# Performance work log

Hardware: AMD Instinct MI355X
Metric: run time of the kernel (lower is better)

Reference implementation:

```python
import jax, jax.numpy as jnp
import numpy as np

B, F, L = 16384, 32, 64
FEAT, DOM, R = 100000, 8, 16
D_IN = F * L  # 2048
N_HIDDEN = 3  # hidden_units = [256, 128, 1]


def _p(k, shape, scale=0.05):
    return jax.random.normal(k, shape, dtype=jnp.float32) * scale


def setup_inputs() -> dict:
    key = jax.random.key(0)
    ks = jax.random.split(key, 32)
    return {
        'x': jax.random.randint(ks[0], (B, F), 0, FEAT),
        'd': jax.random.randint(ks[1], (B,), 0, DOM),
        'emb': _p(ks[2], (FEAT, L)),
        # share MLP: 2048 -> 1024 -> 512 (ReLU after each)
        'sW0': _p(ks[3], (D_IN, 1024)), 'sb0': _p(ks[4], (1024,)),
        'sW1': _p(ks[5], (1024, 512)), 'sb1': _p(ks[6], (512,)),
        # domain layer: 512 -> 256 shared kernel + per-domain LoRA
        'Dk0': _p(ks[7], (512, 256)), 'Db0': _p(ks[8], (256,)),
        'DA0': _p(ks[9], (DOM, 512, R)), 'DB0': _p(ks[10], (DOM, R, 256)), 'Dlb0': _p(ks[11], (DOM, 256)),
        # task layers: 256 -> 128 -> 1 shared kernels + per-task LoRA
        'Tk0': _p(ks[12], (256, 128)), 'Tb0': _p(ks[13], (128,)),
        'Tk1': _p(ks[14], (128, 1)), 'Tb1': _p(ks[15], (1,)),
        'TA0': _p(ks[16], (2, 256, R)), 'TB0': _p(ks[17], (2, R, 128)), 'Tlb0': _p(ks[18], (2, 128)),
        'TA1': _p(ks[19], (2, 128, R)), 'TB1': _p(ks[20], (2, R, 1)), 'Tlb1': _p(ks[21], (2, 1)),
        # gate hypernet + heads
        'gW0': _p(ks[22], (D_IN, 1024)), 'gb0': _p(ks[23], (1024,)),
        'gW1': _p(ks[24], (1024, 512)), 'gb1': _p(ks[25], (512,)),
        'h0W': _p(ks[26], (512, 4)), 'h0b': _p(ks[27], (4,)),
        'h1W': _p(ks[28], (512, 4)), 'h1b': _p(ks[29], (4,)),
    }


def _mlp2(x, W0, b0, W1, b1):
    return jax.nn.relu(jax.nn.relu(x @ W0 + b0) @ W1 + b1)


def _forward(x, d, emb, sW0, sb0, sW1, sb1, Dk0, Db0, DA0, DB0, Dlb0,
             Tk0, Tb0, Tk1, Tb1, TA0, TB0, Tlb0, TA1, TB1, Tlb1,
             gW0, gb0, gW1, gb1, h0W, h0b, h1W, h1b):
    x_emb = emb[x].reshape(x.shape[0], -1)          # (B, dnn_dim)
    x_dnn = _mlp2(x_emb, sW0, sb0, sW1, sb1)        # (B, 512)

    # ---- domain layer (i=0), k=0 -> ReLU applied ----
    share = x_dnn @ Dk0 + Db0                        # (B, 256)
    lora = jnp.einsum('bi,bir->br', x_dnn, DA0[d])   # per-sample domain LoRA gather+matmul
    lora = jnp.einsum('br,bro->bo', lora, DB0[d]) + Dlb0[d]
    d_dnn = jax.nn.relu(share + lora)                # activated
    # d_share / d_lora kept PRE-activation, as in source

    t_dnn = [d_dnn, d_dnn]
    t_share = [share, share]
    t_lora = [lora, lora]
    t_sl, t_ls = [], []
    Tk, Tb = [Tk0, Tk1], [Tb0, Tb1]
    TA, TB, Tlb = [TA0, TA1], [TB0, TB1], [Tlb0, Tlb1]

    k = 1  # shared counter, faithfully incremented per (i, t) step
    for i in range(2):
        for t in range(2):
            ds = t_dnn[t] @ Tk[i] + Tb[i]
            ss = t_share[t] @ Tk[i] + Tb[i]
            ls = t_lora[t] @ Tk[i] + Tb[i]
            t_ls.append(ls)
            A, Bm, lb = TA[i][t], TB[i][t], Tlb[i][t]
            dl = (t_dnn[t] @ A) @ Bm + lb[None, :]
            sl = (t_share[t] @ A) @ Bm + lb[None, :]
            ll = (t_lora[t] @ A) @ Bm + lb[None, :]
            t_dnn[t] = ds + dl
            t_share[t] = ss
            t_lora[t] = ll
            t_sl.append(sl)
            if k + 1 < N_HIDDEN:  # only fires at (i=0, t=0)
                t_dnn[t] = jax.nn.relu(t_dnn[t])
                t_share[t] = jax.nn.relu(t_share[t])
                t_lora[t] = jax.nn.relu(t_lora[t])
                t_sl[t] = jax.nn.relu(t_sl[t])
                t_ls[t] = jax.nn.relu(t_ls[t])
                k += 1

    # ---- gating (hypernet sees detached embedding) ----
    hyper = _mlp2(jax.lax.stop_gradient(x_emb), gW0, gb0, gW1, gb1)
    gates = [jax.nn.sigmoid(hyper @ h0W + h0b), jax.nn.sigmoid(hyper @ h1W + h1b)]

    outs = []
    for t in range(2):
        g = gates[t]
        # t_dnn/t_share/t_lora are (B,1); t_sl[t]/t_ls[t] are (B,128) from i=0 -> broadcast (B,128)
        outs.append(t_dnn[t] - g[:, 0:1] * t_share[t] - g[:, 1:2] * t_lora[t]
                    - g[:, 2:3] * t_sl[t] - g[:, 3:4] * t_ls[t])
    return jnp.stack(outs)  # (2, B, 128)


def reference(x, d, emb, sW0, sb0, sW1, sb1, Dk0, Db0, DA0, DB0, Dlb0,
              Tk0, Tb0, Tk1, Tb1, TA0, TB0, Tlb0, TA1, TB1, Tlb1,
              gW0, gb0, gW1, gb1, h0W, h0b, h1W, h1b):
    return _forward(x, d, emb, sW0, sb0, sW1, sb1, Dk0, Db0, DA0, DB0, Dlb0,
                    Tk0, Tb0, Tk1, Tb1, TA0, TB0, Tlb0, TA1, TB1, Tlb1,
                    gW0, gb0, gW1, gb1, h0W, h0b, h1W, h1b)
```

## Files before the change

kernel.cpp:

```cpp
#include <hip/hip_runtime.h>
#include <hip/hip_bf16.h>

#define BATCH 16384

typedef __attribute__((ext_vector_type(4))) float f32x4;
typedef __attribute__((ext_vector_type(8))) short bf16x8;

__device__ inline float b2f(unsigned short u) {
    union { unsigned u; float f; } c; c.u = ((unsigned)u) << 16; return c.f;
}
__device__ inline unsigned short f2b(float f) {
    __hip_bfloat16 h = __float2bfloat16(f);
    return *(unsigned short*)&h;
}

#define GLL16(g, l)                                                            \
    __builtin_amdgcn_global_load_lds(                                          \
        (const __attribute__((address_space(1))) void*)(g),                    \
        (__attribute__((address_space(3))) void*)(l), 16, 0, 0)

__global__ __launch_bounds__(256) void k_prep(
    const float* __restrict__ sW0, const float* __restrict__ gW0,
    const float* __restrict__ sW1, const float* __restrict__ gW1,
    const float* __restrict__ Dk0, const float* __restrict__ Tk0,
    const float* __restrict__ TA0,
    const float* __restrict__ sb0, const float* __restrict__ gb0,
    const float* __restrict__ sb1, const float* __restrict__ gb1,
    const float* __restrict__ Tb0, const float* __restrict__ DA0,
    const float* __restrict__ DB0, const float* __restrict__ emb,
    unsigned short* __restrict__ W1t, unsigned short* __restrict__ W2cat,
    unsigned short* __restrict__ Dk0t, unsigned short* __restrict__ Tcat,
    float* __restrict__ b1cat, float* __restrict__ b2cat, float* __restrict__ tb0c,
    unsigned short* __restrict__ DA0b, unsigned short* __restrict__ DB0b,
    unsigned short* __restrict__ embB)
{
    int id = blockIdx.x;
    const int tid = threadIdx.x;
    __shared__ float t[32][33];
    auto tcvt = [&](const float* src, int K, int N, unsigned short* dst,
                    int dst_off, int dst_ld, int bx, int by) {
        int k0 = by * 32, n0 = bx * 32;
        int tx = tid & 31, ty = tid >> 5;
        #pragma unroll
        for (int s = 0; s < 32; s += 8) {
            int k = k0 + ty + s, n = n0 + tx;
            t[ty + s][tx] = (k < K && n < N) ? src[(size_t)k * N + n] : 0.f;
        }
        __syncthreads();
        #pragma unroll
        for (int s = 0; s < 32; s += 8) {
            int n = n0 + ty + s, k = k0 + tx;
            if (n < N && k < K)
                dst[(size_t)(dst_off + n) * dst_ld + k] = f2b(t[tx][ty + s]);
        }
    };
    if (id < 4096) { int z = id >> 11, rem = id & 2047;
        tcvt(z ? gW0 : sW0, 2048, 1024, W1t, z * 1024, 2048, rem & 31, rem >> 5); return; }
    id -= 4096;
    if (id < 1024) { int z = id >> 9, rem = id & 511;
        tcvt(z ? gW1 : sW1, 1024, 512, W2cat, z * 512, 1024, rem & 15, rem >> 4); return; }
    id -= 1024;
    if (id < 128) { tcvt(Dk0, 512, 256, Dk0t, 0, 512, id & 7, id >> 3); return; }
    id -= 128;
    if (id < 32)  { tcvt(Tk0, 256, 128, Tcat, 0, 256, id & 3, id >> 2); return; }
    id -= 32;
    if (id < 16)  { int z = id >> 3;
        tcvt(TA0 + z * 256 * 16, 256, 16, Tcat, 128 + z * 16, 256, 0, id & 7); return; }
    id -= 16;
    if (id < 397) {
        int i = id * 256 + tid;
        if (i < 1024)            { b1cat[i] = sb0[i]; return; }
        if (i < 2048)            { b1cat[i] = gb0[i - 1024]; return; }
        if (i < 2560)            { b2cat[i - 2048] = sb1[i - 2048]; return; }
        if (i < 3072)            { b2cat[i - 2560 + 512] = gb1[i - 2560]; return; }
        if (i < 3200)            { tb0c[i - 3072] = Tb0[i - 3072]; return; }
        if (i < 3232)            { tb0c[i - 3200 + 128] = 0.f; return; }
        i -= 3232;
        if (i < 65536)           { DA0b[i] = f2b(DA0[i]); return; }
        i -= 65536;
        if (i < 32768)           { DB0b[i] = f2b(DB0[i]); return; }
        return;
    }
    id -= 397;
    {
        int e = (id * 256 + tid) * 4;
        if (e < 100000 * 64) {
            float4 v = *(const float4*)(emb + e);
            ushort4 o = { f2b(v.x), f2b(v.y), f2b(v.z), f2b(v.w) };
            *(ushort4*)(embB + e) = o;
        }
    }
}

template<int RELU, int OUTBF16, int GATHER>
__global__ __launch_bounds__(512, 2) void k_gemm256(
    const unsigned short* __restrict__ A, int lda, long Az,
    const unsigned short* __restrict__ Bt, int K, long Bz,
    const float* __restrict__ bias, int biasz,
    void* __restrict__ C, int ldc, long Cz,
    int N, const int* __restrict__ xsrc, const unsigned short* __restrict__ embB)
{
    extern __shared__ char smem_raw[];
    const int NT = K >> 6;
    const int tid  = threadIdx.x;
    const int lane = tid & 63;
    const int w    = tid >> 6;
    const int wr   = w >> 2, wc = w & 3;
    const int frow = lane & 15, kg = lane >> 4;
    const int z = blockIdx.z;
    A    += (size_t)z * Az;
    Bt   += (size_t)z * Bz;
    bias += (size_t)z * biasz;

    const int gx  = gridDim.x;
    const int nwg = gx * gridDim.y;
    const int lin = blockIdx.y * gx + blockIdx.x;
    const int qq  = nwg >> 3;
    const int swz = (lin & 7) * qq + (lin >> 3);
    const int bx = swz % gx, by = swz / gx;
    const int row0 = by * 256, col0 = bx * 256;

    const int lch = (lane & 7) ^ ((lane >> 3) & 7);
    const int isA = (lch < 4);
    const int eoBase = lch * 8;
    int* xbT = (int*)(smem_raw + 131072);
    int rrh[4];
    const unsigned short* gsrc[4];
    #pragma unroll
    for (int h = 0; h < 4; ++h) {
        int rr = h * 64 + w * 8 + (lane >> 3);
        rrh[h] = rr;
        if (isA) gsrc[h] = GATHER ? embB : A + (size_t)(row0 + rr) * lda + lch * 8;
        else     gsrc[h] = Bt + (size_t)min(col0 + rr, N - 1) * K + (lch - 4) * 8;
    }
    const int dBase = w * 1024;

    const int pA = (kg ^ (frow & 7)) * 16;
    const int pB = ((4 + kg) ^ (frow & 7)) * 16;
    int aOff[8], bOff[4];
    #pragma unroll
    for (int m = 0; m < 8; ++m) aOff[m] = (wr * 128 + m * 16 + frow) * 128 + pA;
    #pragma unroll
    for (int n = 0; n < 4; ++n) bOff[n] = (wc * 64 + n * 16 + frow) * 128 + pB;

#define STAGE(t_, ks_, slot_) do {                                              \
        int tc_ = min((int)(t_), NT - 1);                                       \
        int o_ = tc_ * 64 + (ks_) * 32;                                         \
        char* d_ = smem_raw + (slot_) * 65536 + (ks_) * 32768 + dBase;          \
        GLL16(gsrc[0] + o_, d_);                                                \
        GLL16(gsrc[1] + o_, d_ + 8192);                                         \
        GLL16(gsrc[2] + o_, d_ + 16384);                                        \
        GLL16(gsrc[3] + o_, d_ + 24576);                                        \
    } while (0)
#define STAGEX(ix_, tcb_, ks_, slot_) do {                                      \
        char* d_ = smem_raw + (slot_) * 65536 + (ks_) * 32768 + dBase;          \
        _Pragma("unroll")                                                       \
        for (int h_ = 0; h_ < 4; ++h_) {                                        \
            const unsigned short* sa_ = embB + (size_t)(ix_)[h_] * 64           \
                                        + (ks_) * 32 + eoBase;                  \
            const unsigned short* sb2_ = gsrc[h_] + (tcb_) * 64 + (ks_) * 32;   \
            GLL16(isA ? sa_ : sb2_, d_ + h_ * 8192);                            \
        }                                                                       \
    } while (0)
#define READS(sb_, ks_) do {                                                    \
        _Pragma("unroll")                                                       \
        for (int n = 0; n < 4; ++n)                                             \
            bfr[n] = *(const bf16x8*)(smem_raw + (sb_) + (ks_) * 32768 + bOff[n]); \
        _Pragma("unroll")                                                       \
        for (int mi = 0; mi < 8; ++mi)                                          \
            afr[mi] = *(const bf16x8*)(smem_raw + (sb_) + (ks_) * 32768 + aOff[mi]); \
    } while (0)
#define MFMA32() do {                                                           \
        __builtin_amdgcn_s_setprio(1);                                          \
        _Pragma("unroll")                                                       \
        for (int mi = 0; mi < 8; ++mi)                                          \
            _Pragma("unroll")                                                   \
            for (int n = 0; n < 4; ++n)                                         \
                acc[mi][n] = __builtin_amdgcn_mfma_f32_16x16x32_bf16(           \
                    bfr[n], afr[mi], acc[mi][n], 0, 0, 0);                      \
        __builtin_amdgcn_s_setprio(0);                                          \
    } while (0)
#define VM4   asm volatile("s_waitcnt vmcnt(4)" ::: "memory")
#define BARM  asm volatile("s_barrier" ::: "memory")

    f32x4 acc[8][4] = {};
    bf16x8 afr[8], bfr[4];
    int ixc[4] = {0, 0, 0, 0};

    if (GATHER) {
        const char* xs = (const char*)(xsrc + row0 * 32);
        #pragma unroll
        for (int r = 0; r < 4; ++r)
            GLL16(xs + r * 8192 + w * 1024 + lane * 16,
                  smem_raw + 65536 + r * 8192 + w * 1024);
        asm volatile("s_waitcnt vmcnt(0)" ::: "memory");
        BARM;
        const int* xlin = (const int*)(smem_raw + 65536);
        #pragma unroll
        for (int r = 0; r < 4; ++r) {
            int i = (r * 512 + tid) * 4;
            int rr_ = i >> 5, tc_ = i & 31;
            int4 vv = *(const int4*)(xlin + i);
            xbT[(tc_ + 0) * 256 + (rr_ ^ ((tc_ + 0) & 31))] = vv.x;
            xbT[(tc_ + 1) * 256 + (rr_ ^ ((tc_ + 1) & 31))] = vv.y;
            xbT[(tc_ + 2) * 256 + (rr_ ^ ((tc_ + 2) & 31))] = vv.z;
            xbT[(tc_ + 3) * 256 + (rr_ ^ ((tc_ + 3) & 31))] = vv.w;
        }
        asm volatile("s_waitcnt lgkmcnt(0)" ::: "memory");
        BARM;
        int ix0[4];
        #pragma unroll
        for (int h = 0; h < 4; ++h) ix0[h] = xbT[rrh[h]];
        STAGEX(ix0, 0, 0, 0); STAGEX(ix0, 0, 1, 0);
        int t1 = min(1, NT - 1);
        #pragma unroll
        for (int h = 0; h < 4; ++h) ixc[h] = xbT[t1 * 256 + (rrh[h] ^ (t1 & 31))];
    } else {
        STAGE(0, 0, 0); STAGE(0, 1, 0);
    }
    VM4; BARM;

    for (int t = 0; t < NT; ++t) {
        const int slot = t & 1, nslot = slot ^ 1;
        const int sb = slot * 65536;
        const int tcn = min(t + 1, NT - 1);
        int ixn[4];
        READS(sb, 0);
        if (GATHER) STAGEX(ixc, tcn, 0, nslot); else STAGE(t + 1, 0, nslot);
        if (GATHER) {
            int tc2 = min(t + 2, NT - 1);
            #pragma unroll
            for (int h = 0; h < 4; ++h) ixn[h] = xbT[tc2 * 256 + (rrh[h] ^ (tc2 & 31))];
        }
        MFMA32();
        VM4; BARM;
        READS(sb, 1);
        if (GATHER) STAGEX(ixc, tcn, 1, nslot); else STAGE(t + 1, 1, nslot);
        MFMA32();
        VM4; BARM;
        if (GATHER) {
            #pragma unroll
            for (int h = 0; h < 4; ++h) ixc[h] = ixn[h];
        }
    }
#undef STAGE
#undef STAGEX
#undef READS
#undef MFMA32
#undef VM4
#undef BARM

    #pragma unroll
    for (int m = 0; m < 8; ++m) {
        int row = row0 + wr * 128 + m * 16 + frow;
        #pragma unroll
        for (int n = 0; n < 4; ++n) {
            int col = col0 + wc * 64 + n * 16 + kg * 4;
            float4 bv = *(const float4*)(bias + col);
            float v0 = acc[m][n][0] + bv.x, v1 = acc[m][n][1] + bv.y;
            float v2 = acc[m][n][2] + bv.z, v3 = acc[m][n][3] + bv.w;
            if (RELU) {
                v0 = fmaxf(v0, 0.f); v1 = fmaxf(v1, 0.f);
                v2 = fmaxf(v2, 0.f); v3 = fmaxf(v3, 0.f);
            }
            if (OUTBF16) {
                ushort4 o = { f2b(v0), f2b(v1), f2b(v2), f2b(v3) };
                *(ushort4*)((unsigned short*)C + (size_t)z * Cz + (size_t)row * ldc + col) = o;
            } else {
                float4 o = { v0, v1, v2, v3 };
                *(float4*)((float*)C + (size_t)z * Cz + (size_t)row * ldc + col) = o;
            }
        }
    }
}

template<int RELU, int OUTBF16>
__global__ __launch_bounds__(256) void k_gemm(
    const unsigned short* __restrict__ A, int lda,
    const unsigned short* __restrict__ Bt,
    const float* __restrict__ bias,
    void* __restrict__ C, int ldc,
    int N, int K)
{
    __shared__ __align__(16) unsigned short As[128 * 32];
    __shared__ __align__(16) unsigned short Bs[128 * 32];
    const int tid  = threadIdx.x;
    const int lane = tid & 63;
    const int w    = tid >> 6;
    const int wr   = w >> 1, wc = w & 1;
    const int row0 = blockIdx.y * 128;
    const int col0 = blockIdx.x * 128;
    const int frow = lane & 15;
    const int kg   = lane >> 4;
    const int sw   = kg ^ ((frow >> 1) & 3);

    const int srow = w * 32 + (lane >> 2);
    const int csw  = (lane & 3) ^ ((lane >> 3) & 3);
    const int br0  = min(col0 + srow, N - 1);
    const int br1  = min(col0 + srow + 16, N - 1);

    const unsigned short* a0 = A  + (size_t)(row0 + srow) * lda      + csw * 8;
    const unsigned short* a1 = A  + (size_t)(row0 + srow + 16) * lda + csw * 8;
    const unsigned short* b0 = Bt + (size_t)br0 * K + csw * 8;
    const unsigned short* b1 = Bt + (size_t)br1 * K + csw * 8;
    unsigned short* lA0 = As + (w * 2 + 0) * 512;
    unsigned short* lA1 = As + (w * 2 + 1) * 512;
    unsigned short* lB0 = Bs + (w * 2 + 0) * 512;
    unsigned short* lB1 = Bs + (w * 2 + 1) * 512;

    f32x4 acc[4][4] = {};

    for (int bk = 0; bk < K; bk += 32) {
        __syncthreads();
        GLL16(a0 + bk, lA0);
        GLL16(a1 + bk, lA1);
        GLL16(b0 + bk, lB0);
        GLL16(b1 + bk, lB1);
        __syncthreads();
        bf16x8 af[4], bfr[4];
        #pragma unroll
        for (int m = 0; m < 4; ++m)
            af[m] = *(const bf16x8*)&As[(wr * 64 + m * 16 + frow) * 32 + sw * 8];
        #pragma unroll
        for (int n = 0; n < 4; ++n)
            bfr[n] = *(const bf16x8*)&Bs[(wc * 64 + n * 16 + frow) * 32 + sw * 8];
        #pragma unroll
        for (int m = 0; m < 4; ++m)
            #pragma unroll
            for (int n = 0; n < 4; ++n)
                acc[m][n] = __builtin_amdgcn_mfma_f32_16x16x32_bf16(bfr[n], af[m], acc[m][n], 0, 0, 0);
    }

    #pragma unroll
    for (int m = 0; m < 4; ++m) {
        int row = row0 + wr * 64 + m * 16 + frow;
        #pragma unroll
        for (int n = 0; n < 4; ++n) {
            int col = col0 + wc * 64 + n * 16 + kg * 4;
            if (col >= N) continue;
            float4 bv = *(const float4*)(bias + col);
            float v0 = acc[m][n][0] + bv.x, v1 = acc[m][n][1] + bv.y;
            float v2 = acc[m][n][2] + bv.z, v3 = acc[m][n][3] + bv.w;
            if (RELU) {
                v0 = fmaxf(v0, 0.f); v1 = fmaxf(v1, 0.f);
                v2 = fmaxf(v2, 0.f); v3 = fmaxf(v3, 0.f);
            }
            if (OUTBF16) {
                ushort4 o = { f2b(v0), f2b(v1), f2b(v2), f2b(v3) };
                *(ushort4*)((unsigned short*)C + (size_t)row * ldc + col) = o;
            } else {
                float4 o = { v0, v1, v2, v3 };
                *(float4*)((float*)C + (size_t)row * ldc + col) = o;
            }
        }
    }
}

__global__ __launch_bounds__(256) void k_dlora(
    const unsigned short* __restrict__ Xdnn, const int* __restrict__ d,
    const unsigned short* __restrict__ DA0b, const unsigned short* __restrict__ DB0b,
    const float* __restrict__ Dlb0,
    const unsigned short* __restrict__ SHARE,
    unsigned short* __restrict__ LORA, unsigned short* __restrict__ DDNN)
{
    int w = threadIdx.x >> 6, lane = threadIdx.x & 63;
    int b = blockIdx.x * 4 + w;
    int dom = d[b];
    uint4 raw = *(const uint4*)(Xdnn + (size_t)b * 512 + lane * 8);
    const unsigned short* pr = (const unsigned short*)&raw;
    float xv[8];
    #pragma unroll
    for (int j = 0; j < 8; ++j) xv[j] = b2f(pr[j]);

    const unsigned short* Ap = DA0b + ((size_t)dom * 512 + lane * 8) * 16;
    float v[16];
    #pragma unroll
    for (int r = 0; r < 16; ++r) v[r] = 0.f;
    #pragma unroll
    for (int j = 0; j < 8; ++j) {
        uint4 a0 = *(const uint4*)(Ap + j * 16);
        uint4 a1 = *(const uint4*)(Ap + j * 16 + 8);
        const unsigned short* ap = (const unsigned short*)&a0;
        const unsigned short* aq = (const unsigned short*)&a1;
        float xj = xv[j];
        #pragma unroll
        for (int r = 0; r < 8; ++r) v[r]     += xj * b2f(ap[r]);
        #pragma unroll
        for (int r = 0; r < 8; ++r) v[r + 8] += xj * b2f(aq[r]);
    }
    #pragma unroll
    for (int s = 1; s < 64; s <<= 1) {
        #pragma unroll
        for (int r = 0; r < 16; ++r) v[r] += __shfl_xor(v[r], s, 64);
    }
    const unsigned short* Bp = DB0b + (size_t)dom * 16 * 256;
    const float* lbp = Dlb0 + (size_t)dom * 256;
    #pragma unroll
    for (int c = 0; c < 4; ++c) {
        int o = lane + c * 64;
        float a = lbp[o];
        #pragma unroll
        for (int r = 0; r < 16; ++r) a += v[r] * b2f(Bp[r * 256 + o]);
        float sh = b2f(SHARE[(size_t)b * 256 + o]);
        LORA[(size_t)b * 256 + o] = f2b(a);
        DDNN[(size_t)b * 256 + o] = f2b(fmaxf(sh + a, 0.f));
    }
}

__global__ __launch_bounds__(256) void k_tail(
    const float* __restrict__ Yd, const float* __restrict__ Ys, const float* __restrict__ Yl,
    const unsigned short* __restrict__ Hyper,
    const float* __restrict__ TB0, const float* __restrict__ Tlb0,
    const float* __restrict__ Tk1, const float* __restrict__ Tb1,
    const float* __restrict__ TA1, const float* __restrict__ TB1, const float* __restrict__ Tlb1,
    const float* __restrict__ h0W, const float* __restrict__ h0b,
    const float* __restrict__ h1W, const float* __restrict__ h1b,
    float* __restrict__ out)
{
    __shared__ float sTB0[2][16][128];
    __shared__ float sTlb0[2][128];
    __shared__ float sTk1[128];
    __shared__ float sWeff[2][128];
    __shared__ float sY[4][3][160];
    const int tid = threadIdx.x;

    for (int i = tid; i < 4096; i += 256) ((float*)sTB0)[i] = TB0[i];
    if (tid < 256) ((float*)sTlb0)[tid] = Tlb0[tid];
    if (tid < 128) sTk1[tid] = Tk1[tid];
    {
        int t = tid >> 7, j = tid & 127;
        float a = 0.f;
        #pragma unroll
        for (int r = 0; r < 16; ++r) a += TA1[((size_t)t * 128 + j) * 16 + r] * TB1[t * 16 + r];
        sWeff[t][j] = a;
    }
    const float* Yp[3] = {Yd, Ys, Yl};
    int b0 = blockIdx.x * 4;
    for (int i = tid; i < 4 * 3 * 160; i += 256) {
        int s = i / 480, rem = i % 480, st = rem / 160, idx = rem % 160;
        sY[s][st][idx] = Yp[st][(size_t)(b0 + s) * 160 + idx];
    }
    __syncthreads();

    int w = tid >> 6, lane = tid & 63;
    int b = b0 + w;
    const float* yd = sY[w][0];
    const float* ys = sY[w][1];
    const float* yl = sY[w][2];
    int j0 = lane, j1 = lane + 64;

    uint4 hraw = *(const uint4*)(Hyper + (size_t)b * 512 + lane * 8);
    const unsigned short* hp = (const unsigned short*)&hraw;
    float hv[8];
    #pragma unroll
    for (int j = 0; j < 8; ++j) hv[j] = b2f(hp[j]);

    float red[14];
    #pragma unroll
    for (int k = 0; k < 14; ++k) red[k] = 0.f;
    #pragma unroll
    for (int j = 0; j < 8; ++j) {
        float4 w0 = *(const float4*)(h0W + (size_t)(lane * 8 + j) * 4);
        float4 w1 = *(const float4*)(h1W + (size_t)(lane * 8 + j) * 4);
        red[0] += hv[j] * w0.x; red[1] += hv[j] * w0.y; red[2] += hv[j] * w0.z; red[3] += hv[j] * w0.w;
        red[4] += hv[j] * w1.x; red[5] += hv[j] * w1.y; red[6] += hv[j] * w1.z; red[7] += hv[j] * w1.w;
    }

    float SLv[2][2], LSv[2][2];
    #pragma unroll
    for (int t = 0; t < 2; ++t) {
        float lb0 = sTlb0[t][j0], lb1 = sTlb0[t][j1];
        float dl0 = lb0, dl1 = lb1, sl0 = lb0, sl1 = lb1, ll0 = lb0, ll1 = lb1;
        #pragma unroll
        for (int r = 0; r < 16; ++r) {
            float w0v = sTB0[t][r][j0], w1v = sTB0[t][r][j1];
            float ud = yd[128 + t * 16 + r];
            float us = ys[128 + t * 16 + r];
            float ul = yl[128 + t * 16 + r];
            dl0 += ud * w0v; dl1 += ud * w1v;
            sl0 += us * w0v; sl1 += us * w1v;
            ll0 += ul * w0v; ll1 += ul * w1v;
        }
        float D0 = yd[j0] + dl0, D1 = yd[j1] + dl1;
        float S0 = ys[j0],       S1 = ys[j1];
        float L0 = ll0,          L1 = ll1;
        float sl_0 = sl0, sl_1 = sl1;
        float ls_0 = yl[j0], ls_1 = yl[j1];
        if (t == 0) {
            D0 = fmaxf(D0, 0.f); D1 = fmaxf(D1, 0.f);
            S0 = fmaxf(S0, 0.f); S1 = fmaxf(S1, 0.f);
            L0 = fmaxf(L0, 0.f); L1 = fmaxf(L1, 0.f);
            sl_0 = fmaxf(sl_0, 0.f); sl_1 = fmaxf(sl_1, 0.f);
            ls_0 = fmaxf(ls_0, 0.f); ls_1 = fmaxf(ls_1, 0.f);
        }
        SLv[t][0] = sl_0; SLv[t][1] = sl_1;
        LSv[t][0] = ls_0; LSv[t][1] = ls_1;
        float we0 = sWeff[t][j0], we1 = sWeff[t][j1];
        float tk0 = sTk1[j0],     tk1v = sTk1[j1];
        red[8 + t * 3 + 0] = D0 * (tk0 + we0) + D1 * (tk1v + we1);
        red[8 + t * 3 + 1] = S0 * tk0 + S1 * tk1v;
        red[8 + t * 3 + 2] = L0 * we0 + L1 * we1;
    }

    #pragma unroll
    for (int s = 1; s < 64; s <<= 1) {
        #pragma unroll
        for (int k = 0; k < 14; ++k) red[k] += __shfl_xor(red[k], s, 64);
    }

    float Tb1v = Tb1[0];
    #pragma unroll
    for (int t = 0; t < 2; ++t) {
        float fd = red[8 + t * 3 + 0] + Tb1v + Tlb1[t];
        float fs = red[8 + t * 3 + 1] + Tb1v;
        float fl = red[8 + t * 3 + 2] + Tlb1[t];
        const float* hb = t ? h1b : h0b;
        float g0 = 1.f / (1.f + expf(-(red[t * 4 + 0] + hb[0])));
        float g1 = 1.f / (1.f + expf(-(red[t * 4 + 1] + hb[1])));
        float g2 = 1.f / (1.f + expf(-(red[t * 4 + 2] + hb[2])));
        float g3 = 1.f / (1.f + expf(-(red[t * 4 + 3] + hb[3])));
        float base = fd - g0 * fs - g1 * fl;
        size_t o = (size_t)t * BATCH * 128 + (size_t)b * 128;
        out[o + j0] = base - g2 * SLv[t][0] - g3 * LSv[t][0];
        out[o + j1] = base - g2 * SLv[t][1] - g3 * LSv[t][1];
    }
}

extern "C" void kernel_launch(void* const* d_in, const int* in_sizes, int n_in,
                              void* d_out, int out_size, void* d_ws, size_t ws_size,
                              hipStream_t stream)
{
    const int*   x    = (const int*)  d_in[0];
    const int*   dix  = (const int*)  d_in[1];
    const float* emb  = (const float*)d_in[2];
    const float* sW0  = (const float*)d_in[3];
    const float* sb0  = (const float*)d_in[4];
    const float* sW1  = (const float*)d_in[5];
    const float* sb1  = (const float*)d_in[6];
    const float* Dk0  = (const float*)d_in[7];
    const float* Db0  = (const float*)d_in[8];
    const float* DA0  = (const float*)d_in[9];
    const float* DB0  = (const float*)d_in[10];
    const float* Dlb0 = (const float*)d_in[11];
    const float* Tk0  = (const float*)d_in[12];
    const float* Tb0  = (const float*)d_in[13];
    const float* Tk1  = (const float*)d_in[14];
    const float* Tb1  = (const float*)d_in[15];
    const float* TA0  = (const float*)d_in[16];
    const float* TB0  = (const float*)d_in[17];
    const float* Tlb0 = (const float*)d_in[18];
    const float* TA1  = (const float*)d_in[19];
    const float* TB1  = (const float*)d_in[20];
    const float* Tlb1 = (const float*)d_in[21];
    const float* gW0  = (const float*)d_in[22];
    const float* gb0  = (const float*)d_in[23];
    const float* gW1  = (const float*)d_in[24];
    const float* gb1  = (const float*)d_in[25];
    const float* h0W  = (const float*)d_in[26];
    const float* h0b  = (const float*)d_in[27];
    const float* h1W  = (const float*)d_in[28];
    const float* h1b  = (const float*)d_in[29];

    hipFuncSetAttribute((const void*)k_gemm256<1, 1, 1>,
                        hipFuncAttributeMaxDynamicSharedMemorySize, 163840);
    hipFuncSetAttribute((const void*)k_gemm256<1, 1, 0>,
                        hipFuncAttributeMaxDynamicSharedMemorySize, 131072);

    char* ws = (char*)d_ws;
    size_t off = 0;
    auto alloc = [&](size_t bytes) -> void* {
        void* p = ws + off;
        off += (bytes + 255) & ~(size_t)255;
        return p;
    };
    unsigned short* W1t   = (unsigned short*)alloc((size_t)2048 * 2048 * 2);
    unsigned short* W2cat = (unsigned short*)alloc((size_t)1024 * 1024 * 2);
    unsigned short* Dk0t  = (unsigned short*)alloc((size_t)256 * 512 * 2);
    unsigned short* Tcat  = (unsigned short*)alloc((size_t)160 * 256 * 2);
    unsigned short* DA0b  = (unsigned short*)alloc((size_t)8 * 512 * 16 * 2);
    unsigned short* DB0b  = (unsigned short*)alloc((size_t)8 * 16 * 256 * 2);
    unsigned short* embB  = (unsigned short*)alloc((size_t)100000 * 64 * 2);
    float*          b1cat = (float*)alloc(2048 * 4);
    float*          b2cat = (float*)alloc(1024 * 4);
    float*          tb0c  = (float*)alloc(160 * 4);
    float*          Ybase = (float*)alloc((size_t)3 * BATCH * 160 * 4);
    char* regB = (char*)alloc((size_t)BATCH * 2048 * 2);
    unsigned short* Xdnn  = (unsigned short*)alloc((size_t)BATCH * 512 * 2);
    unsigned short* Hyper = (unsigned short*)alloc((size_t)BATCH * 512 * 2);

    float* Ys = Ybase;
    float* Yl = Ybase + (size_t)BATCH * 160;
    float* Yd = Ybase + (size_t)2 * BATCH * 160;
    unsigned short* Hbuf  = (unsigned short*)regB;
    unsigned short* SHARE = (unsigned short*)regB;
    unsigned short* LORA  = SHARE + (size_t)BATCH * 256;
    unsigned short* DDNN  = LORA  + (size_t)BATCH * 256;

    k_prep<<<11943, 256, 0, stream>>>(
        sW0, gW0, sW1, gW1, Dk0, Tk0, TA0,
        sb0, gb0, sb1, gb1, Tb0, DA0, DB0, emb,
        W1t, W2cat, Dk0t, Tcat, b1cat, b2cat, tb0c, DA0b, DB0b, embB);

    k_gemm256<1, 1, 1><<<dim3(8, 64, 1), 512, 163840, stream>>>(
        embB, 0, 0, W1t, 2048, 0, b1cat, 0, Hbuf, 2048, 0, 2048, x, embB);
    k_gemm256<1, 1, 0><<<dim3(2, 64, 2), 512, 131072, stream>>>(
        Hbuf, 2048, 1024, W2cat, 1024, (long)512 * 1024, b2cat, 512,
        Xdnn, 512, (long)BATCH * 512, 512, nullptr, nullptr);
    k_gemm<0, 1><<<dim3(2, 128), 256, 0, stream>>>(Xdnn, 512, Dk0t, Db0, SHARE, 256, 256, 512);
    k_dlora<<<BATCH / 4, 256, 0, stream>>>(Xdnn, dix, DA0b, DB0b, Dlb0, SHARE, LORA, DDNN);
    k_gemm<0, 0><<<dim3(2, 384), 256, 0, stream>>>(SHARE, 256, Tcat, tb0c, Ybase, 160, 160, 256);
    k_tail<<<BATCH / 4, 256, 0, stream>>>(Yd, Ys, Yl, Hyper, TB0, Tlb0, Tk1, Tb1,
                                          TA1, TB1, Tlb1, h0W, h0b, h1W, h1b, (float*)d_out);
}
```

Baseline: 344.7 us.

## Fold domain LoRA A-projection into share GEMM, bf16 intermediates, direct index loads

```diff
diff --git a/kernel.cpp b/kernel.cpp
--- a/kernel.cpp
+++ b/kernel.cpp
@@ -26,12 +26,13 @@
     const float* __restrict__ TA0,
     const float* __restrict__ sb0, const float* __restrict__ gb0,
     const float* __restrict__ sb1, const float* __restrict__ gb1,
-    const float* __restrict__ Tb0, const float* __restrict__ DA0,
-    const float* __restrict__ DB0, const float* __restrict__ emb,
+    const float* __restrict__ Tb0, const float* __restrict__ Db0,
+    const float* __restrict__ DA0, const float* __restrict__ DB0,
+    const float* __restrict__ emb,
     unsigned short* __restrict__ W1t, unsigned short* __restrict__ W2cat,
-    unsigned short* __restrict__ Dk0t, unsigned short* __restrict__ Tcat,
+    unsigned short* __restrict__ D3cat, unsigned short* __restrict__ Tcat,
     float* __restrict__ b1cat, float* __restrict__ b2cat, float* __restrict__ tb0c,
-    unsigned short* __restrict__ DA0b, unsigned short* __restrict__ DB0b,
+    float* __restrict__ d3bias, unsigned short* __restrict__ DB0b,
     unsigned short* __restrict__ embB)
 {
     int id = blockIdx.x;
@@ -60,14 +61,17 @@
     if (id < 1024) { int z = id >> 9, rem = id & 511;
         tcvt(z ? gW1 : sW1, 1024, 512, W2cat, z * 512, 1024, rem & 15, rem >> 4); return; }
     id -= 1024;
-    if (id < 128) { tcvt(Dk0, 512, 256, Dk0t, 0, 512, id & 7, id >> 3); return; }
+    if (id < 128) { tcvt(Dk0, 512, 256, D3cat, 0, 512, id & 7, id >> 3); return; }
+    id -= 128;
+    if (id < 128) { int dom = id >> 4, by = id & 15;
+        tcvt(DA0 + (size_t)dom * 512 * 16, 512, 16, D3cat, 256 + dom * 16, 512, 0, by); return; }
     id -= 128;
     if (id < 32)  { tcvt(Tk0, 256, 128, Tcat, 0, 256, id & 3, id >> 2); return; }
     id -= 32;
     if (id < 16)  { int z = id >> 3;
         tcvt(TA0 + z * 256 * 16, 256, 16, Tcat, 128 + z * 16, 256, 0, id & 7); return; }
     id -= 16;
-    if (id < 397) {
+    if (id < 143) {
         int i = id * 256 + tid;
         if (i < 1024)            { b1cat[i] = sb0[i]; return; }
         if (i < 2048)            { b1cat[i] = gb0[i - 1024]; return; }
@@ -75,13 +79,13 @@
         if (i < 3072)            { b2cat[i - 2560 + 512] = gb1[i - 2560]; return; }
         if (i < 3200)            { tb0c[i - 3072] = Tb0[i - 3072]; return; }
         if (i < 3232)            { tb0c[i - 3200 + 128] = 0.f; return; }
-        i -= 3232;
-        if (i < 65536)           { DA0b[i] = f2b(DA0[i]); return; }
-        i -= 65536;
+        if (i < 3488)            { d3bias[i - 3232] = Db0[i - 3232]; return; }
+        if (i < 3616)            { d3bias[i - 3488 + 256] = 0.f; return; }
+        i -= 3616;
         if (i < 32768)           { DB0b[i] = f2b(DB0[i]); return; }
         return;
     }
-    id -= 397;
+    id -= 143;
     {
         int e = (id * 256 + tid) * 4;
         if (e < 100000 * 64) {
@@ -123,7 +127,6 @@
     const int lch = (lane & 7) ^ ((lane >> 3) & 7);
     const int isA = (lch < 4);
     const int eoBase = lch * 8;
-    int* xbT = (int*)(smem_raw + 131072);
     int rrh[4];
     const unsigned short* gsrc[4];
     #pragma unroll
@@ -181,6 +184,7 @@
         __builtin_amdgcn_s_setprio(0);                                          \
     } while (0)
 #define VM4   asm volatile("s_waitcnt vmcnt(4)" ::: "memory")
+#define VM8   asm volatile("s_waitcnt vmcnt(8)" ::: "memory")
 #define BARM  asm volatile("s_barrier" ::: "memory")
 
     f32x4 acc[8][4] = {};
@@ -188,33 +192,13 @@
     int ixc[4] = {0, 0, 0, 0};
 
     if (GATHER) {
-        const char* xs = (const char*)(xsrc + row0 * 32);
-        #pragma unroll
-        for (int r = 0; r < 4; ++r)
-            GLL16(xs + r * 8192 + w * 1024 + lane * 16,
-                  smem_raw + 65536 + r * 8192 + w * 1024);
-        asm volatile("s_waitcnt vmcnt(0)" ::: "memory");
-        BARM;
-        const int* xlin = (const int*)(smem_raw + 65536);
-        #pragma unroll
-        for (int r = 0; r < 4; ++r) {
-            int i = (r * 512 + tid) * 4;
-            int rr_ = i >> 5, tc_ = i & 31;
-            int4 vv = *(const int4*)(xlin + i);
-            xbT[(tc_ + 0) * 256 + (rr_ ^ ((tc_ + 0) & 31))] = vv.x;
-            xbT[(tc_ + 1) * 256 + (rr_ ^ ((tc_ + 1) & 31))] = vv.y;
-            xbT[(tc_ + 2) * 256 + (rr_ ^ ((tc_ + 2) & 31))] = vv.z;
-            xbT[(tc_ + 3) * 256 + (rr_ ^ ((tc_ + 3) & 31))] = vv.w;
-        }
-        asm volatile("s_waitcnt lgkmcnt(0)" ::: "memory");
-        BARM;
         int ix0[4];
         #pragma unroll
-        for (int h = 0; h < 4; ++h) ix0[h] = xbT[rrh[h]];
+        for (int h = 0; h < 4; ++h) ix0[h] = xsrc[(row0 + rrh[h]) * 32];
+        int t1 = min(1, NT - 1);
+        #pragma unroll
+        for (int h = 0; h < 4; ++h) ixc[h] = xsrc[(row0 + rrh[h]) * 32 + t1];
         STAGEX(ix0, 0, 0, 0); STAGEX(ix0, 0, 1, 0);
-        int t1 = min(1, NT - 1);
-        #pragma unroll
-        for (int h = 0; h < 4; ++h) ixc[h] = xbT[t1 * 256 + (rrh[h] ^ (t1 & 31))];
     } else {
         STAGE(0, 0, 0); STAGE(0, 1, 0);
     }
@@ -230,14 +214,16 @@
         if (GATHER) {
             int tc2 = min(t + 2, NT - 1);
             #pragma unroll
-            for (int h = 0; h < 4; ++h) ixn[h] = xbT[tc2 * 256 + (rrh[h] ^ (tc2 & 31))];
+            for (int h = 0; h < 4; ++h) ixn[h] = xsrc[(row0 + rrh[h]) * 32 + tc2];
         }
         MFMA32();
-        VM4; BARM;
+        if (GATHER) VM8; else VM4;
+        BARM;
         READS(sb, 1);
         if (GATHER) STAGEX(ixc, tcn, 1, nslot); else STAGE(t + 1, 1, nslot);
         MFMA32();
-        VM4; BARM;
+        if (GATHER) VM8; else VM4;
+        BARM;
         if (GATHER) {
             #pragma unroll
             for (int h = 0; h < 4; ++h) ixc[h] = ixn[h];
@@ -248,6 +234,7 @@
 #undef READS
 #undef MFMA32
 #undef VM4
+#undef VM8
 #undef BARM
 
     #pragma unroll
@@ -356,43 +343,23 @@
     }
 }
 
-__global__ __launch_bounds__(256) void k_dlora(
-    const unsigned short* __restrict__ Xdnn, const int* __restrict__ d,
-    const unsigned short* __restrict__ DA0b, const unsigned short* __restrict__ DB0b,
-    const float* __restrict__ Dlb0,
-    const unsigned short* __restrict__ SHARE,
+__global__ __launch_bounds__(256) void k_dlora2(
+    const unsigned short* __restrict__ SHV, const int* __restrict__ d,
+    const unsigned short* __restrict__ DB0b, const float* __restrict__ Dlb0,
+    unsigned short* __restrict__ SHARE,
     unsigned short* __restrict__ LORA, unsigned short* __restrict__ DDNN)
 {
     int w = threadIdx.x >> 6, lane = threadIdx.x & 63;
     int b = blockIdx.x * 4 + w;
     int dom = d[b];
-    uint4 raw = *(const uint4*)(Xdnn + (size_t)b * 512 + lane * 8);
-    const unsigned short* pr = (const unsigned short*)&raw;
-    float xv[8];
-    #pragma unroll
-    for (int j = 0; j < 8; ++j) xv[j] = b2f(pr[j]);
-
-    const unsigned short* Ap = DA0b + ((size_t)dom * 512 + lane * 8) * 16;
+    const unsigned short* vp = SHV + (size_t)b * 384 + 256 + dom * 16;
+    uint4 v0 = *(const uint4*)vp;
+    uint4 v1 = *(const uint4*)(vp + 8);
+    const unsigned short* pv0 = (const unsigned short*)&v0;
+    const unsigned short* pv1 = (const unsigned short*)&v1;
     float v[16];
     #pragma unroll
-    for (int r = 0; r < 16; ++r) v[r] = 0.f;
-    #pragma unroll
-    for (int j = 0; j < 8; ++j) {
-        uint4 a0 = *(const uint4*)(Ap + j * 16);
-        uint4 a1 = *(const uint4*)(Ap + j * 16 + 8);
-        const unsigned short* ap = (const unsigned short*)&a0;
-        const unsigned short* aq = (const unsigned short*)&a1;
-        float xj = xv[j];
-        #pragma unroll
-        for (int r = 0; r < 8; ++r) v[r]     += xj * b2f(ap[r]);
-        #pragma unroll
-        for (int r = 0; r < 8; ++r) v[r + 8] += xj * b2f(aq[r]);
-    }
-    #pragma unroll
-    for (int s = 1; s < 64; s <<= 1) {
-        #pragma unroll
-        for (int r = 0; r < 16; ++r) v[r] += __shfl_xor(v[r], s, 64);
-    }
+    for (int r = 0; r < 8; ++r) { v[r] = b2f(pv0[r]); v[r + 8] = b2f(pv1[r]); }
     const unsigned short* Bp = DB0b + (size_t)dom * 16 * 256;
     const float* lbp = Dlb0 + (size_t)dom * 256;
     #pragma unroll
@@ -401,14 +368,17 @@
         float a = lbp[o];
         #pragma unroll
         for (int r = 0; r < 16; ++r) a += v[r] * b2f(Bp[r * 256 + o]);
-        float sh = b2f(SHARE[(size_t)b * 256 + o]);
+        unsigned short shb = SHV[(size_t)b * 384 + o];
+        float sh = b2f(shb);
+        SHARE[(size_t)b * 256 + o] = shb;
         LORA[(size_t)b * 256 + o] = f2b(a);
         DDNN[(size_t)b * 256 + o] = f2b(fmaxf(sh + a, 0.f));
     }
 }
 
 __global__ __launch_bounds__(256) void k_tail(
-    const float* __restrict__ Yd, const float* __restrict__ Ys, const float* __restrict__ Yl,
+    const unsigned short* __restrict__ Yd, const unsigned short* __restrict__ Ys,
+    const unsigned short* __restrict__ Yl,
     const unsigned short* __restrict__ Hyper,
     const float* __restrict__ TB0, const float* __restrict__ Tlb0,
     const float* __restrict__ Tk1, const float* __restrict__ Tb1,
@@ -434,11 +404,11 @@
         for (int r = 0; r < 16; ++r) a += TA1[((size_t)t * 128 + j) * 16 + r] * TB1[t * 16 + r];
         sWeff[t][j] = a;
     }
-    const float* Yp[3] = {Yd, Ys, Yl};
+    const unsigned short* Yp[3] = {Yd, Ys, Yl};
     int b0 = blockIdx.x * 4;
     for (int i = tid; i < 4 * 3 * 160; i += 256) {
         int s = i / 480, rem = i % 480, st = rem / 160, idx = rem % 160;
-        sY[s][st][idx] = Yp[st][(size_t)(b0 + s) * 160 + idx];
+        sY[s][st][idx] = b2f(Yp[st][(size_t)(b0 + s) * 160 + idx]);
     }
     __syncthreads();
 
@@ -562,7 +532,7 @@
     const float* h1b  = (const float*)d_in[29];
 
     hipFuncSetAttribute((const void*)k_gemm256<1, 1, 1>,
-                        hipFuncAttributeMaxDynamicSharedMemorySize, 163840);
+                        hipFuncAttributeMaxDynamicSharedMemorySize, 131072);
     hipFuncSetAttribute((const void*)k_gemm256<1, 1, 0>,
                         hipFuncAttributeMaxDynamicSharedMemorySize, 131072);
 
@@ -575,40 +545,41 @@
     };
     unsigned short* W1t   = (unsigned short*)alloc((size_t)2048 * 2048 * 2);
     unsigned short* W2cat = (unsigned short*)alloc((size_t)1024 * 1024 * 2);
-    unsigned short* Dk0t  = (unsigned short*)alloc((size_t)256 * 512 * 2);
+    unsigned short* D3cat = (unsigned short*)alloc((size_t)384 * 512 * 2);
     unsigned short* Tcat  = (unsigned short*)alloc((size_t)160 * 256 * 2);
-    unsigned short* DA0b  = (unsigned short*)alloc((size_t)8 * 512 * 16 * 2);
     unsigned short* DB0b  = (unsigned short*)alloc((size_t)8 * 16 * 256 * 2);
     unsigned short* embB  = (unsigned short*)alloc((size_t)100000 * 64 * 2);
     float*          b1cat = (float*)alloc(2048 * 4);
     float*          b2cat = (float*)alloc(1024 * 4);
     float*          tb0c  = (float*)alloc(160 * 4);
-    float*          Ybase = (float*)alloc((size_t)3 * BATCH * 160 * 4);
+    float*          d3bias= (float*)alloc(384 * 4);
+    unsigned short* SHV   = (unsigned short*)alloc((size_t)BATCH * 384 * 2);
+    unsigned short* Ybase = (unsigned short*)alloc((size_t)3 * BATCH * 160 * 2);
     char* regB = (char*)alloc((size_t)BATCH * 2048 * 2);
     unsigned short* Xdnn  = (unsigned short*)alloc((size_t)BATCH * 512 * 2);
     unsigned short* Hyper = (unsigned short*)alloc((size_t)BATCH * 512 * 2);
 
-    float* Ys = Ybase;
-    float* Yl = Ybase + (size_t)BATCH * 160;
-    float* Yd = Ybase + (size_t)2 * BATCH * 160;
+    unsigned short* Ys = Ybase;
+    unsigned short* Yl = Ybase + (size_t)BATCH * 160;
+    unsigned short* Yd = Ybase + (size_t)2 * BATCH * 160;
     unsigned short* Hbuf  = (unsigned short*)regB;
     unsigned short* SHARE = (unsigned short*)regB;
     unsigned short* LORA  = SHARE + (size_t)BATCH * 256;
     unsigned short* DDNN  = LORA  + (size_t)BATCH * 256;
 
-    k_prep<<<11943, 256, 0, stream>>>(
+    k_prep<<<11817, 256, 0, stream>>>(
         sW0, gW0, sW1, gW1, Dk0, Tk0, TA0,
-        sb0, gb0, sb1, gb1, Tb0, DA0, DB0, emb,
-        W1t, W2cat, Dk0t, Tcat, b1cat, b2cat, tb0c, DA0b, DB0b, embB);
-
-    k_gemm256<1, 1, 1><<<dim3(8, 64, 1), 512, 163840, stream>>>(
+        sb0, gb0, sb1, gb1, Tb0, Db0, DA0, DB0, emb,
+        W1t, W2cat, D3cat, Tcat, b1cat, b2cat, tb0c, d3bias, DB0b, embB);
+
+    k_gemm256<1, 1, 1><<<dim3(8, 64, 1), 512, 131072, stream>>>(
         embB, 0, 0, W1t, 2048, 0, b1cat, 0, Hbuf, 2048, 0, 2048, x, embB);
     k_gemm256<1, 1, 0><<<dim3(2, 64, 2), 512, 131072, stream>>>(
         Hbuf, 2048, 1024, W2cat, 1024, (long)512 * 1024, b2cat, 512,
         Xdnn, 512, (long)BATCH * 512, 512, nullptr, nullptr);
-    k_gemm<0, 1><<<dim3(2, 128), 256, 0, stream>>>(Xdnn, 512, Dk0t, Db0, SHARE, 256, 256, 512);
-    k_dlora<<<BATCH / 4, 256, 0, stream>>>(Xdnn, dix, DA0b, DB0b, Dlb0, SHARE, LORA, DDNN);
-    k_gemm<0, 0><<<dim3(2, 384), 256, 0, stream>>>(SHARE, 256, Tcat, tb0c, Ybase, 160, 160, 256);
+    k_gemm<0, 1><<<dim3(3, 128), 256, 0, stream>>>(Xdnn, 512, D3cat, d3bias, SHV, 384, 384, 512);
+    k_dlora2<<<BATCH / 4, 256, 0, stream>>>(SHV, dix, DB0b, Dlb0, SHARE, LORA, DDNN);
+    k_gemm<0, 1><<<dim3(2, 384), 256, 0, stream>>>(SHARE, 256, Tcat, tb0c, Ybase, 160, 160, 256);
     k_tail<<<BATCH / 4, 256, 0, stream>>>(Yd, Ys, Yl, Hyper, TB0, Tlb0, Tk1, Tb1,
                                           TA1, TB1, Tlb1, h0W, h0b, h1W, h1b, (float*)d_out);
 }
```

Result: faster. 320.5 us (-7.0%).
